# Kernel tuning notes

Measured on AMD Instinct MI355X. Metric: run time of the kernel, lower is better.

The kernel has to match this reference:

```python
import jax, jax.numpy as jnp
import numpy as np

EMB = 1024
HEADS = 16
HEAD_DIM = EMB // HEADS
FF = 4 * EMB
B, S = 4, 2048


def gelu_tanh(x):
    c = jnp.sqrt(jnp.asarray(2.0 / jnp.pi, x.dtype))
    return 0.5 * x * (1.0 + jnp.tanh(c * (x + 0.044715 * x ** 3)))


def layernorm(x, g, b, eps=1e-5):
    mu = jnp.mean(x, axis=-1, keepdims=True)
    var = jnp.var(x, axis=-1, keepdims=True)
    return (x - mu) * jax.lax.rsqrt(var + eps) * g + b


def setup_inputs() -> dict:
    key = jax.random.key(0)
    ks = jax.random.split(key, 12)
    s = 0.02
    return {
        "x": jax.random.normal(ks[0], (B, S, EMB), jnp.float32),
        "Wq": jax.random.normal(ks[1], (EMB, EMB), jnp.float32) * s,
        "bq": jnp.zeros((EMB,), jnp.float32),
        "Wk": jax.random.normal(ks[2], (EMB, EMB), jnp.float32) * s,
        "bk": jnp.zeros((EMB,), jnp.float32),
        "Wv": jax.random.normal(ks[3], (EMB, EMB), jnp.float32) * s,
        "bv": jnp.zeros((EMB,), jnp.float32),
        "Wo": jax.random.normal(ks[4], (EMB, EMB), jnp.float32) * s,
        "bo": jnp.zeros((EMB,), jnp.float32),
        "W1": jax.random.normal(ks[5], (EMB, FF), jnp.float32) * s,
        "b1": jnp.zeros((FF,), jnp.float32),
        "W2": jax.random.normal(ks[6], (FF, EMB), jnp.float32) * s,
        "b2": jnp.zeros((EMB,), jnp.float32),
        "g1": jnp.ones((EMB,), jnp.float32),
        "be1": jnp.zeros((EMB,), jnp.float32),
        "g2": jnp.ones((EMB,), jnp.float32),
        "be2": jnp.zeros((EMB,), jnp.float32),
    }


def reference(x, Wq, bq, Wk, bk, Wv, bv, Wo, bo, W1, b1, W2, b2, g1, be1, g2, be2):
    b, s, _ = x.shape
    shortcut = x
    h = layernorm(x, g1, be1)
    # QKV projections -> [b, heads, s, head_dim]
    def proj(W, bias):
        return (h @ W + bias).reshape(b, s, HEADS, HEAD_DIM).transpose(0, 2, 1, 3)
    q, k, v = proj(Wq, bq), proj(Wk, bk), proj(Wv, bv)
    scores = jnp.einsum('bhqd,bhkd->bhqk', q, k) / jnp.sqrt(jnp.asarray(HEAD_DIM, x.dtype))
    causal = jnp.triu(jnp.ones((s, s), bool), k=1)  # True above diagonal -> masked
    scores = jnp.where(causal, -jnp.inf, scores)
    probs = jax.nn.softmax(scores, axis=-1)  # dropout p=0 -> identity
    ctx = jnp.einsum('bhqk,bhkd->bhqd', probs, v).transpose(0, 2, 1, 3).reshape(b, s, EMB)
    attn_out = ctx @ Wo + bo
    x = attn_out + shortcut
    shortcut = x
    h = layernorm(x, g2, be2)
    ff = gelu_tanh(h @ W1 + b1) @ W2 + b2
    return ff + shortcut
```

## Files before the change

kernel.cpp:

```cpp
#include <hip/hip_runtime.h>
#include <hip/hip_bf16.h>

#define EMB 1024
#define HEADS 16
#define HDIM 64
#define FFDIM 4096
#define BSZ 4
#define SEQ 2048
#define MROWS (BSZ * SEQ)
#define QKVW 3072
#define VSTRIDE 2080

typedef __attribute__((ext_vector_type(8))) short bf16x8;
typedef __attribute__((ext_vector_type(4))) float f32x4;
typedef __attribute__((ext_vector_type(16))) float f32x16;
typedef __attribute__((ext_vector_type(4))) unsigned short u16x4;
typedef unsigned short u16;

__device__ __forceinline__ float bf2f(u16 u) {
  union { unsigned int i; float f; } c; c.i = ((unsigned int)u) << 16; return c.f;
}
__device__ __forceinline__ u16 f2bf(float f) {
  union { float f; unsigned int i; } c; c.f = f;
  unsigned int i = c.i + 0x7fff + ((c.i >> 16) & 1);
  return (u16)(i >> 16);
}
__device__ __forceinline__ unsigned fbits(float f) {
  union { float f; unsigned u; } c; c.f = f; return c.u;
}
__device__ __forceinline__ unsigned pk2(float e0, float e1) {
  return (fbits(e0) >> 16) | (fbits(e1) & 0xffff0000u);
}
__device__ __forceinline__ f32x16 zero16() {
  f32x16 z;
#pragma unroll
  for (int i = 0; i < 16; ++i) z[i] = 0.f;
  return z;
}
__device__ __forceinline__ void gload16(const u16* g, void* lds) {
  __builtin_amdgcn_global_load_lds(
      (const __attribute__((address_space(1))) void*)g,
      (__attribute__((address_space(3))) void*)lds, 16, 0, 0);
}

__global__ __launch_bounds__(256) void ln_kernel(
    const float* __restrict__ x, const float* __restrict__ g,
    const float* __restrict__ be, u16* __restrict__ out) {
  int w = threadIdx.x >> 6, l = threadIdx.x & 63;
  size_t row = (size_t)blockIdx.x * 4 + w;
  const float* xr = x + row * EMB;
  float f[4][4];
  float s = 0.f, s2 = 0.f;
#pragma unroll
  for (int c = 0; c < 4; ++c) {
    f32x4 v = *(const f32x4*)(xr + c * 256 + l * 4);
#pragma unroll
    for (int j = 0; j < 4; ++j) {
      f[c][j] = v[j];
      s += v[j];
      s2 += v[j] * v[j];
    }
  }
#pragma unroll
  for (int m = 1; m < 64; m <<= 1) {
    s  += __shfl_xor(s, m);
    s2 += __shfl_xor(s2, m);
  }
  float mu = s * (1.f / EMB);
  float var = s2 * (1.f / EMB) - mu * mu;
  float rs = rsqrtf(var + 1e-5f);
#pragma unroll
  for (int c = 0; c < 4; ++c) {
    u16x4 o;
#pragma unroll
    for (int j = 0; j < 4; ++j) {
      int col = c * 256 + l * 4 + j;
      o[j] = f2bf((f[c][j] - mu) * rs * g[col] + be[col]);
    }
    *(u16x4*)(out + row * EMB + c * 256 + l * 4) = o;
  }
}

__global__ __launch_bounds__(256) void transpose_cvt(
    const float* __restrict__ in, u16* __restrict__ out, int R, int C) {
  __shared__ u16 tile[32][33];
  int c0 = blockIdx.x * 32, r0 = blockIdx.y * 32;
  int tx = threadIdx.x, ty = threadIdx.y;
#pragma unroll
  for (int i = ty; i < 32; i += 8)
    tile[i][tx] = f2bf(in[(size_t)(r0 + i) * C + c0 + tx]);
  __syncthreads();
#pragma unroll
  for (int i = ty; i < 32; i += 8)
    out[(size_t)(c0 + i) * R + r0 + tx] = tile[tx][i];
}

__global__ __launch_bounds__(256) void concat_bias(
    const float* __restrict__ a, const float* __restrict__ b,
    const float* __restrict__ c, float* __restrict__ o) {
  int i = blockIdx.x * 256 + threadIdx.x;
  o[i] = i < 1024 ? a[i] : (i < 2048 ? b[i - 1024] : c[i - 2048]);
}

__global__ __launch_bounds__(256) void transpose_v(
    const u16* __restrict__ QKV, u16* __restrict__ Vt) {
  __shared__ u16 tile[32][33];
  int s0 = blockIdx.x * 32, d0 = blockIdx.y * 32, bh = blockIdx.z;
  int h = bh % HEADS, b = bh / HEADS;
  int tx = threadIdx.x, ty = threadIdx.y;
  const u16* src = QKV + (size_t)b * SEQ * QKVW + 2048 + h * HDIM;
  u16* dst = Vt + (size_t)bh * HDIM * VSTRIDE;
#pragma unroll
  for (int i = ty; i < 32; i += 8)
    tile[i][tx] = src[(size_t)(s0 + i) * QKVW + d0 + tx];
  __syncthreads();
#pragma unroll
  for (int i = ty; i < 32; i += 8)
    dst[(size_t)(d0 + i) * VSTRIDE + s0 + tx] = tile[tx][i];
}

__device__ __forceinline__ float gelu_f(float v) {
  float u = 1.5957691216057308f * (v + 0.044715f * v * v * v);
  return v / (1.f + __expf(-u));
}

template <int EPI, typename OT>
__global__ __launch_bounds__(256, 3) void gemm32(
    const u16* __restrict__ A, const u16* __restrict__ Bt,
    const float* __restrict__ bias, const float* __restrict__ res,
    OT* __restrict__ C, int N, int K) {
  __shared__ char lds[16384];
  int nbn = N >> 7;
  int cpx = gridDim.x >> 3;
  int bid = blockIdx.x;
  int logical = (bid & 7) * cpx + (bid >> 3);
  int mb = logical / nbn, nb = logical % nbn;
  int m0 = mb << 7, n0 = nb << 7;
  int t = threadIdx.x, w = t >> 6, l = t & 63;
  int wr = w >> 1, wc = w & 1;
  int l31 = l & 31, lh = l >> 5;
  int srow = (w << 4) + (l >> 2);
  int scol = (((l & 3) ^ ((srow >> 1) & 3)) << 3);
  char* dstA = lds + (w << 10);
  char* dstB = lds + 8192 + (w << 10);

  f32x16 acc[2][2] = {{zero16(), zero16()}, {zero16(), zero16()}};

  for (int k0 = 0; k0 < K; k0 += 32) {
    __syncthreads();
    gload16(A + (size_t)(m0 + srow) * K + k0 + scol, dstA);
    gload16(A + (size_t)(m0 + 64 + srow) * K + k0 + scol, dstA + 4096);
    gload16(Bt + (size_t)(n0 + srow) * K + k0 + scol, dstB);
    gload16(Bt + (size_t)(n0 + 64 + srow) * K + k0 + scol, dstB + 4096);
    __syncthreads();
    bf16x8 afr[2][2], bfr[2][2];
#pragma unroll
    for (int blk = 0; blk < 2; ++blk)
#pragma unroll
      for (int kk = 0; kk < 2; ++kk) {
        int ra = (wr << 6) + (blk << 5) + l31;
        int rb = (wc << 6) + (blk << 5) + l31;
        int pa = (((kk << 1) + lh) ^ ((ra >> 1) & 3)) << 4;
        int pb = (((kk << 1) + lh) ^ ((rb >> 1) & 3)) << 4;
        afr[blk][kk] = *(const bf16x8*)(lds + ra * 64 + pa);
        bfr[blk][kk] = *(const bf16x8*)(lds + 8192 + rb * 64 + pb);
      }
#pragma unroll
    for (int m = 0; m < 2; ++m)
#pragma unroll
      for (int n = 0; n < 2; ++n)
#pragma unroll
        for (int kk = 0; kk < 2; ++kk)
          acc[m][n] = __builtin_amdgcn_mfma_f32_32x32x16_bf16(
              afr[m][kk], bfr[n][kk], acc[m][n], 0, 0, 0);
  }

#pragma unroll
  for (int m = 0; m < 2; ++m)
#pragma unroll
    for (int n = 0; n < 2; ++n) {
      int col = n0 + (wc << 6) + (n << 5) + l31;
      float bcol = bias[col];
      int rbase = m0 + (wr << 6) + (m << 5) + (lh << 2);
#pragma unroll
      for (int reg = 0; reg < 16; ++reg) {
        int row = rbase + (reg & 3) + ((reg >> 2) << 3);
        float v = acc[m][n][reg] + bcol;
        if (EPI & 2) v = gelu_f(v);
        if (EPI & 1) v += res[(size_t)row * N + col];
        if (sizeof(OT) == 2)
          C[(size_t)row * N + col] = (OT)f2bf(v);
        else
          C[(size_t)row * N + col] = (OT)v;
      }
    }
}

#define QKT32(ACCS, QF)                                                     \
  do {                                                                      \
    ACCS = zero16();                                                        \
    _Pragma("unroll") for (int s_ = 0; s_ < 4; ++s_)                        \
        ACCS = __builtin_amdgcn_mfma_f32_32x32x16_bf16(kf[s_], QF[s_],      \
                                                       ACCS, 0, 0, 0);      \
  } while (0)

#define ATTN_STEP(ACCS, M, L, O0, O1, DIAG)                                 \
  do {                                                                      \
    float e_[16];                                                           \
    float tm = -1e30f;                                                      \
    _Pragma("unroll") for (int i = 0; i < 16; ++i) {                        \
      float sv = ACCS[i];                                                   \
      if (DIAG) {                                                           \
        int kvl = (i & 3) + 8 * (i >> 2) + 4 * g;                           \
        if (kvl > lq) sv = -1e30f;                                          \
      }                                                                     \
      e_[i] = sv;                                                           \
      tm = fmaxf(tm, sv);                                                   \
    }                                                                       \
    tm = fmaxf(tm, __shfl_xor(tm, 32));                                     \
    float nm = fmaxf(M, tm);                                                \
    if (!__all(tm <= M)) {                                                  \
      float scl = __expf(M - nm);                                           \
      L *= scl;                                                             \
      _Pragma("unroll") for (int i = 0; i < 16; ++i) {                      \
        O0[i] *= scl;                                                       \
        O1[i] *= scl;                                                       \
      }                                                                     \
    }                                                                       \
    M = nm;                                                                 \
    float ts = 0.f;                                                         \
    _Pragma("unroll") for (int i = 0; i < 16; ++i) {                        \
      e_[i] = __expf(e_[i] - nm);                                           \
      ts += e_[i];                                                          \
    }                                                                       \
    ts += __shfl_xor(ts, 32);                                               \
    L += ts;                                                                \
    _Pragma("unroll") for (int s_ = 0; s_ < 2; ++s_) {                      \
      unsigned plo0 = pk2(e_[8 * s_ + 0], e_[8 * s_ + 1]);                  \
      unsigned plo1 = pk2(e_[8 * s_ + 2], e_[8 * s_ + 3]);                  \
      unsigned phi0 = pk2(e_[8 * s_ + 4], e_[8 * s_ + 5]);                  \
      unsigned phi1 = pk2(e_[8 * s_ + 6], e_[8 * s_ + 7]);                  \
      unsigned recv0 = __shfl_xor(g ? plo0 : phi0, 32);                     \
      unsigned recv1 = __shfl_xor(g ? plo1 : phi1, 32);                     \
      union { unsigned u[4]; bf16x8 v; } pf_;                               \
      pf_.u[0] = g ? recv0 : plo0;                                          \
      pf_.u[1] = g ? recv1 : plo1;                                          \
      pf_.u[2] = g ? phi0 : recv0;                                          \
      pf_.u[3] = g ? phi1 : recv1;                                          \
      O0 = __builtin_amdgcn_mfma_f32_32x32x16_bf16(vf[0][s_], pf_.v, O0,    \
                                                   0, 0, 0);                \
      O1 = __builtin_amdgcn_mfma_f32_32x32x16_bf16(vf[1][s_], pf_.v, O1,    \
                                                   0, 0, 0);                \
    }                                                                       \
  } while (0)

#define LOAD_KV(KV0)                                                        \
  do {                                                                      \
    _Pragma("unroll") for (int s_ = 0; s_ < 4; ++s_)                        \
        kf[s_] = *(const bf16x8*)(Kp + (size_t)((KV0) + lq) * QKVW +        \
                                  s_ * 16 + g * 8);                         \
    _Pragma("unroll") for (int d_ = 0; d_ < 2; ++d_)                        \
        _Pragma("unroll") for (int s_ = 0; s_ < 2; ++s_)                    \
            vf[d_][s_] = *(const bf16x8*)(Vt +                              \
                (size_t)(d_ * 32 + lq) * VSTRIDE + (KV0) + s_ * 16 + g * 8);\
  } while (0)

#define WRITE_OUT(O0, O1, L, WQ0)                                           \
  do {                                                                      \
    float inv = 1.f / L;                                                    \
    u16* orow = Op + (size_t)((WQ0) + lq) * EMB;                            \
    _Pragma("unroll") for (int dblk = 0; dblk < 2; ++dblk) {                \
      _Pragma("unroll") for (int p = 0; p < 8; ++p) {                       \
        int i0 = 2 * p;                                                     \
        int d = dblk * 32 + 2 * (p & 1) + 8 * (p >> 1) + 4 * g;             \
        float v0 = (dblk ? O1[i0] : O0[i0]) * inv;                          \
        float v1 = (dblk ? O1[i0 + 1] : O0[i0 + 1]) * inv;                  \
        unsigned wd = (unsigned)f2bf(v0) | ((unsigned)f2bf(v1) << 16);      \
        *(unsigned*)(orow + d) = wd;                                        \
      }                                                                     \
    }                                                                       \
  } while (0)

__global__ __launch_bounds__(256, 2) void attn_kernel(
    const u16* __restrict__ QKV, const u16* __restrict__ VtG,
    u16* __restrict__ O) {
  int t = threadIdx.x, w = t >> 6, l = t & 63;
  int lq = l & 31, g = l >> 5;
  int wid = blockIdx.x * 4 + w;
  int qi = wid & 31, bh = wid >> 5;
  int h = bh & (HEADS - 1), b = bh >> 4;
  int wq0a = qi * 32, wq0b = (63 - qi) * 32;
  int ntA = qi + 1, ntB = 64 - qi;
  const u16* Qp = QKV + (size_t)b * SEQ * QKVW + h * HDIM;
  const u16* Kp = QKV + (size_t)b * SEQ * QKVW + 1024 + h * HDIM;
  const u16* Vt = VtG + (size_t)bh * HDIM * VSTRIDE;
  u16* Op = O + (size_t)b * SEQ * EMB + h * HDIM;

  bf16x8 qfA[4], qfB[4];
#pragma unroll
  for (int s = 0; s < 4; ++s) {
    bf16x8 ra = *(const bf16x8*)(Qp + (size_t)(wq0a + lq) * QKVW + s * 16 + g * 8);
    bf16x8 rb = *(const bf16x8*)(Qp + (size_t)(wq0b + lq) * QKVW + s * 16 + g * 8);
#pragma unroll
    for (int j = 0; j < 8; ++j) {
      qfA[s][j] = (short)f2bf(bf2f((u16)ra[j]) * 0.125f);
      qfB[s][j] = (short)f2bf(bf2f((u16)rb[j]) * 0.125f);
    }
  }

  f32x16 oA0 = zero16(), oA1 = zero16(), oB0 = zero16(), oB1 = zero16();
  f32x16 sA, sB;
  float mA = -1e30f, lA = 0.f, mB = -1e30f, lB = 0.f;
  bf16x8 kf[4], vf[2][2];

  for (int ti = 0; ti < ntA; ++ti) {
    int kv0 = ti * 32;
    LOAD_KV(kv0);
    QKT32(sA, qfA);
    QKT32(sB, qfB);
    bool diagA = (ti == ntA - 1);
    ATTN_STEP(sA, mA, lA, oA0, oA1, diagA);
    ATTN_STEP(sB, mB, lB, oB0, oB1, false);
  }
  WRITE_OUT(oA0, oA1, lA, wq0a);
  for (int ti = ntA; ti < ntB; ++ti) {
    int kv0 = ti * 32;
    LOAD_KV(kv0);
    QKT32(sB, qfB);
    bool diagB = (ti == ntB - 1);
    ATTN_STEP(sB, mB, lB, oB0, oB1, diagB);
  }
  WRITE_OUT(oB0, oB1, lB, wq0b);
}

extern "C" void kernel_launch(void* const* d_in, const int* in_sizes, int n_in,
                              void* d_out, int out_size, void* d_ws, size_t ws_size,
                              hipStream_t stream) {
  (void)in_sizes; (void)n_in; (void)out_size; (void)ws_size;
  const float* x   = (const float*)d_in[0];
  const float* Wq  = (const float*)d_in[1];
  const float* bq  = (const float*)d_in[2];
  const float* Wk  = (const float*)d_in[3];
  const float* bk  = (const float*)d_in[4];
  const float* Wv  = (const float*)d_in[5];
  const float* bv  = (const float*)d_in[6];
  const float* Wo  = (const float*)d_in[7];
  const float* bo  = (const float*)d_in[8];
  const float* W1  = (const float*)d_in[9];
  const float* b1  = (const float*)d_in[10];
  const float* W2  = (const float*)d_in[11];
  const float* b2  = (const float*)d_in[12];
  const float* g1  = (const float*)d_in[13];
  const float* be1 = (const float*)d_in[14];
  const float* g2  = (const float*)d_in[15];
  const float* be2 = (const float*)d_in[16];

  char* ws = (char*)d_ws;
  const size_t MB = 1ull << 20;
  u16*   WqkvT = (u16*)(ws + 0 * MB);
  u16*   WoT   = (u16*)(ws + 6 * MB);
  u16*   W1T   = (u16*)(ws + 8 * MB);
  u16*   W2T   = (u16*)(ws + 16 * MB);
  float* bqkv  = (float*)(ws + 24 * MB);
  u16*   hbuf  = (u16*)(ws + 25 * MB);
  float* x1f   = (float*)(ws + 41 * MB);
  u16*   qkv   = (u16*)(ws + 73 * MB);
  u16*   VtG   = (u16*)(ws + 121 * MB);
  u16*   gbuf  = (u16*)(ws + 73 * MB);

  dim3 tb(32, 8);
  transpose_cvt<<<dim3(EMB / 32, EMB / 32), tb, 0, stream>>>(Wq, WqkvT, EMB, EMB);
  transpose_cvt<<<dim3(EMB / 32, EMB / 32), tb, 0, stream>>>(Wk, WqkvT + 1024 * 1024, EMB, EMB);
  transpose_cvt<<<dim3(EMB / 32, EMB / 32), tb, 0, stream>>>(Wv, WqkvT + 2 * 1024 * 1024, EMB, EMB);
  transpose_cvt<<<dim3(EMB / 32, EMB / 32), tb, 0, stream>>>(Wo, WoT, EMB, EMB);
  transpose_cvt<<<dim3(FFDIM / 32, EMB / 32), tb, 0, stream>>>(W1, W1T, EMB, FFDIM);
  transpose_cvt<<<dim3(EMB / 32, FFDIM / 32), tb, 0, stream>>>(W2, W2T, FFDIM, EMB);
  concat_bias<<<12, 256, 0, stream>>>(bq, bk, bv, bqkv);

  ln_kernel<<<MROWS / 4, 256, 0, stream>>>(x, g1, be1, hbuf);

  gemm32<0, u16><<<(MROWS / 128) * (QKVW / 128), 256, 0, stream>>>(
      hbuf, WqkvT, bqkv, nullptr, qkv, QKVW, EMB);

  transpose_v<<<dim3(SEQ / 32, HDIM / 32, BSZ * HEADS), tb, 0, stream>>>(qkv, VtG);

  attn_kernel<<<BSZ * HEADS * (SEQ / 64) / 4, 256, 0, stream>>>(qkv, VtG, hbuf);

  gemm32<1, float><<<(MROWS / 128) * (EMB / 128), 256, 0, stream>>>(
      hbuf, WoT, bo, x, x1f, EMB, EMB);

  ln_kernel<<<MROWS / 4, 256, 0, stream>>>(x1f, g2, be2, hbuf);

  gemm32<2, u16><<<(MROWS / 128) * (FFDIM / 128), 256, 0, stream>>>(
      hbuf, W1T, b1, nullptr, gbuf, FFDIM, EMB);
  gemm32<1, float><<<(MROWS / 128) * (EMB / 128), 256, 0, stream>>>(
      gbuf, W2T, b2, x1f, (float*)d_out, EMB, FFDIM);
}
```

Baseline: 454.1 us.

## Restructure attention to one query tile per wave with double-buffered KV loads

Replaces the paired causal query tiles per wave (short plus long tile sharing K/V loads) with one 32-row query tile per wave, doubling the grid. K/V fragments are ping-pong double-buffered so the next tile's loads are issued before the current tile's MFMAs, s_setprio is raised around MFMA bursts, and launch bounds go to 3 waves per SIMD. This trades K/V load sharing between two tiles and built-in load balance for lower register pressure, more occupancy and load/compute overlap. Work per wave becomes uneven (1 to 64 tiles), which may create tail imbalance.

```diff
diff --git a/kernel.cpp b/kernel.cpp
--- a/kernel.cpp
+++ b/kernel.cpp
@@ -196,15 +196,17 @@
     }
 }
 
-#define QKT32(ACCS, QF)                                                     \
+#define QKT32A(ACCS, KF)                                                    \
   do {                                                                      \
     ACCS = zero16();                                                        \
+    __builtin_amdgcn_s_setprio(1);                                          \
     _Pragma("unroll") for (int s_ = 0; s_ < 4; ++s_)                        \
-        ACCS = __builtin_amdgcn_mfma_f32_32x32x16_bf16(kf[s_], QF[s_],      \
+        ACCS = __builtin_amdgcn_mfma_f32_32x32x16_bf16(KF[s_], qf[s_],      \
                                                        ACCS, 0, 0, 0);      \
+    __builtin_amdgcn_s_setprio(0);                                          \
   } while (0)
 
-#define ATTN_STEP(ACCS, M, L, O0, O1, DIAG)                                 \
+#define ATTN_STEPA(ACCS, VF, DIAG)                                          \
   do {                                                                      \
     float e_[16];                                                           \
     float tm = -1e30f;                                                      \
@@ -218,23 +220,23 @@
       tm = fmaxf(tm, sv);                                                   \
     }                                                                       \
     tm = fmaxf(tm, __shfl_xor(tm, 32));                                     \
-    float nm = fmaxf(M, tm);                                                \
-    if (!__all(tm <= M)) {                                                  \
-      float scl = __expf(M - nm);                                           \
-      L *= scl;                                                             \
+    float nm = fmaxf(mrun, tm);                                             \
+    if (!__all(tm <= mrun)) {                                               \
+      float scl = __expf(mrun - nm);                                        \
+      lrun *= scl;                                                          \
       _Pragma("unroll") for (int i = 0; i < 16; ++i) {                      \
-        O0[i] *= scl;                                                       \
-        O1[i] *= scl;                                                       \
+        o0[i] *= scl;                                                       \
+        o1[i] *= scl;                                                       \
       }                                                                     \
     }                                                                       \
-    M = nm;                                                                 \
+    mrun = nm;                                                              \
     float ts = 0.f;                                                         \
     _Pragma("unroll") for (int i = 0; i < 16; ++i) {                        \
       e_[i] = __expf(e_[i] - nm);                                           \
       ts += e_[i];                                                          \
     }                                                                       \
     ts += __shfl_xor(ts, 32);                                               \
-    L += ts;                                                                \
+    lrun += ts;                                                             \
     _Pragma("unroll") for (int s_ = 0; s_ < 2; ++s_) {                      \
       unsigned plo0 = pk2(e_[8 * s_ + 0], e_[8 * s_ + 1]);                  \
       unsigned plo1 = pk2(e_[8 * s_ + 2], e_[8 * s_ + 3]);                  \
@@ -247,90 +249,89 @@
       pf_.u[1] = g ? recv1 : plo1;                                          \
       pf_.u[2] = g ? phi0 : recv0;                                          \
       pf_.u[3] = g ? phi1 : recv1;                                          \
-      O0 = __builtin_amdgcn_mfma_f32_32x32x16_bf16(vf[0][s_], pf_.v, O0,    \
+      __builtin_amdgcn_s_setprio(1);                                        \
+      o0 = __builtin_amdgcn_mfma_f32_32x32x16_bf16(VF##0[s_], pf_.v, o0,    \
                                                    0, 0, 0);                \
-      O1 = __builtin_amdgcn_mfma_f32_32x32x16_bf16(vf[1][s_], pf_.v, O1,    \
+      o1 = __builtin_amdgcn_mfma_f32_32x32x16_bf16(VF##1[s_], pf_.v, o1,    \
                                                    0, 0, 0);                \
+      __builtin_amdgcn_s_setprio(0);                                        \
     }                                                                       \
   } while (0)
 
-#define LOAD_KV(KV0)                                                        \
+#define LOAD_KVA(KF, VF, KV0)                                               \
   do {                                                                      \
     _Pragma("unroll") for (int s_ = 0; s_ < 4; ++s_)                        \
-        kf[s_] = *(const bf16x8*)(Kp + (size_t)((KV0) + lq) * QKVW +        \
+        KF[s_] = *(const bf16x8*)(Kp + (size_t)((KV0) + lq) * QKVW +        \
                                   s_ * 16 + g * 8);                         \
-    _Pragma("unroll") for (int d_ = 0; d_ < 2; ++d_)                        \
-        _Pragma("unroll") for (int s_ = 0; s_ < 2; ++s_)                    \
-            vf[d_][s_] = *(const bf16x8*)(Vt +                              \
-                (size_t)(d_ * 32 + lq) * VSTRIDE + (KV0) + s_ * 16 + g * 8);\
+    _Pragma("unroll") for (int s_ = 0; s_ < 2; ++s_) {                      \
+      VF##0[s_] = *(const bf16x8*)(Vt + (size_t)lq * VSTRIDE + (KV0) +      \
+                                   s_ * 16 + g * 8);                        \
+      VF##1[s_] = *(const bf16x8*)(Vt + (size_t)(32 + lq) * VSTRIDE +       \
+                                   (KV0) + s_ * 16 + g * 8);                \
+    }                                                                       \
   } while (0)
 
-#define WRITE_OUT(O0, O1, L, WQ0)                                           \
-  do {                                                                      \
-    float inv = 1.f / L;                                                    \
-    u16* orow = Op + (size_t)((WQ0) + lq) * EMB;                            \
-    _Pragma("unroll") for (int dblk = 0; dblk < 2; ++dblk) {                \
-      _Pragma("unroll") for (int p = 0; p < 8; ++p) {                       \
-        int i0 = 2 * p;                                                     \
-        int d = dblk * 32 + 2 * (p & 1) + 8 * (p >> 1) + 4 * g;             \
-        float v0 = (dblk ? O1[i0] : O0[i0]) * inv;                          \
-        float v1 = (dblk ? O1[i0 + 1] : O0[i0 + 1]) * inv;                  \
-        unsigned wd = (unsigned)f2bf(v0) | ((unsigned)f2bf(v1) << 16);      \
-        *(unsigned*)(orow + d) = wd;                                        \
-      }                                                                     \
-    }                                                                       \
-  } while (0)
-
-__global__ __launch_bounds__(256, 2) void attn_kernel(
+__global__ __launch_bounds__(256, 3) void attn_kernel(
     const u16* __restrict__ QKV, const u16* __restrict__ VtG,
     u16* __restrict__ O) {
   int t = threadIdx.x, w = t >> 6, l = t & 63;
   int lq = l & 31, g = l >> 5;
   int wid = blockIdx.x * 4 + w;
-  int qi = wid & 31, bh = wid >> 5;
+  int qi = wid & 63, bh = wid >> 6;
   int h = bh & (HEADS - 1), b = bh >> 4;
-  int wq0a = qi * 32, wq0b = (63 - qi) * 32;
-  int ntA = qi + 1, ntB = 64 - qi;
+  int wq0 = (63 - qi) * 32;
+  int nt = 64 - qi;
   const u16* Qp = QKV + (size_t)b * SEQ * QKVW + h * HDIM;
   const u16* Kp = QKV + (size_t)b * SEQ * QKVW + 1024 + h * HDIM;
   const u16* Vt = VtG + (size_t)bh * HDIM * VSTRIDE;
   u16* Op = O + (size_t)b * SEQ * EMB + h * HDIM;
 
-  bf16x8 qfA[4], qfB[4];
+  bf16x8 qf[4];
 #pragma unroll
   for (int s = 0; s < 4; ++s) {
-    bf16x8 ra = *(const bf16x8*)(Qp + (size_t)(wq0a + lq) * QKVW + s * 16 + g * 8);
-    bf16x8 rb = *(const bf16x8*)(Qp + (size_t)(wq0b + lq) * QKVW + s * 16 + g * 8);
-#pragma unroll
-    for (int j = 0; j < 8; ++j) {
-      qfA[s][j] = (short)f2bf(bf2f((u16)ra[j]) * 0.125f);
-      qfB[s][j] = (short)f2bf(bf2f((u16)rb[j]) * 0.125f);
+    bf16x8 r = *(const bf16x8*)(Qp + (size_t)(wq0 + lq) * QKVW + s * 16 + g * 8);
+#pragma unroll
+    for (int j = 0; j < 8; ++j)
+      qf[s][j] = (short)f2bf(bf2f((u16)r[j]) * 0.125f);
+  }
+
+  f32x16 o0 = zero16(), o1 = zero16(), s;
+  float mrun = -1e30f, lrun = 0.f;
+  bf16x8 kfA[4], vfA0[2], vfA1[2], kfB[4], vfB0[2], vfB1[2];
+
+  LOAD_KVA(kfA, vfA, 0);
+  int ti = 0;
+  while (ti + 2 <= nt) {
+    LOAD_KVA(kfB, vfB, (ti + 1) * 32);
+    QKT32A(s, kfA);
+    ATTN_STEPA(s, vfA, false);
+    bool diagB = (ti + 2 == nt);
+    if (ti + 2 < nt) LOAD_KVA(kfA, vfA, (ti + 2) * 32);
+    QKT32A(s, kfB);
+    ATTN_STEPA(s, vfB, diagB);
+    ti += 2;
+  }
+  if (ti < nt) {
+    QKT32A(s, kfA);
+    ATTN_STEPA(s, vfA, true);
+  }
+
+  {
+    float inv = 1.f / lrun;
+    u16* orow = Op + (size_t)(wq0 + lq) * EMB;
+#pragma unroll
+    for (int dblk = 0; dblk < 2; ++dblk) {
+#pragma unroll
+      for (int p = 0; p < 8; ++p) {
+        int i0 = 2 * p;
+        int d = dblk * 32 + 2 * (p & 1) + 8 * (p >> 1) + 4 * g;
+        float v0 = (dblk ? o1[i0] : o0[i0]) * inv;
+        float v1 = (dblk ? o1[i0 + 1] : o0[i0 + 1]) * inv;
+        unsigned wd = (unsigned)f2bf(v0) | ((unsigned)f2bf(v1) << 16);
+        *(unsigned*)(orow + d) = wd;
+      }
     }
   }
-
-  f32x16 oA0 = zero16(), oA1 = zero16(), oB0 = zero16(), oB1 = zero16();
-  f32x16 sA, sB;
-  float mA = -1e30f, lA = 0.f, mB = -1e30f, lB = 0.f;
-  bf16x8 kf[4], vf[2][2];
-
-  for (int ti = 0; ti < ntA; ++ti) {
-    int kv0 = ti * 32;
-    LOAD_KV(kv0);
-    QKT32(sA, qfA);
-    QKT32(sB, qfB);
-    bool diagA = (ti == ntA - 1);
-    ATTN_STEP(sA, mA, lA, oA0, oA1, diagA);
-    ATTN_STEP(sB, mB, lB, oB0, oB1, false);
-  }
-  WRITE_OUT(oA0, oA1, lA, wq0a);
-  for (int ti = ntA; ti < ntB; ++ti) {
-    int kv0 = ti * 32;
-    LOAD_KV(kv0);
-    QKT32(sB, qfB);
-    bool diagB = (ti == ntB - 1);
-    ATTN_STEP(sB, mB, lB, oB0, oB1, diagB);
-  }
-  WRITE_OUT(oB0, oB1, lB, wq0b);
 }
 
 extern "C" void kernel_launch(void* const* d_in, const int* in_sizes, int n_in,
@@ -384,7 +385,7 @@
 
   transpose_v<<<dim3(SEQ / 32, HDIM / 32, BSZ * HEADS), tb, 0, stream>>>(qkv, VtG);
 
-  attn_kernel<<<BSZ * HEADS * (SEQ / 64) / 4, 256, 0, stream>>>(qkv, VtG, hbuf);
+  attn_kernel<<<BSZ * HEADS * (SEQ / 32) / 4, 256, 0, stream>>>(qkv, VtG, hbuf);
 
   gemm32<1, float><<<(MROWS / 128) * (EMB / 128), 256, 0, stream>>>(
       hbuf, WoT, bo, x, x1f, EMB, EMB);
```

New measurement: 539.6 us. 18.8% more time.

## Split attention KV range across wave pairs and double GEMM K-step

Applied to the files above, without the earlier changes.

The attention kernel now gives each query-tile pair to two waves that each process half of the KV tiles, then merges the partial softmax states through shared memory, doubling the grid and raising the occupancy hint. MFMA sections are wrapped in s_setprio raises. Separately, the GEMM loads a 64-wide K slab per iteration with an 8-way XOR swizzle, halving the barrier count at the cost of twice the LDS per block. The extra merge step, the shared-memory footprint and the larger LDS could reduce occupancy.

```diff
diff --git a/kernel.cpp b/kernel.cpp
--- a/kernel.cpp
+++ b/kernel.cpp
@@ -129,7 +129,9 @@
     const u16* __restrict__ A, const u16* __restrict__ Bt,
     const float* __restrict__ bias, const float* __restrict__ res,
     OT* __restrict__ C, int N, int K) {
-  __shared__ char lds[16384];
+  __shared__ char lds[32768];
+  char* ldsA = lds;
+  char* ldsB = lds + 16384;
   int nbn = N >> 7;
   int cpx = gridDim.x >> 3;
   int bid = blockIdx.x;
@@ -139,40 +141,44 @@
   int t = threadIdx.x, w = t >> 6, l = t & 63;
   int wr = w >> 1, wc = w & 1;
   int l31 = l & 31, lh = l >> 5;
-  int srow = (w << 4) + (l >> 2);
-  int scol = (((l & 3) ^ ((srow >> 1) & 3)) << 3);
-  char* dstA = lds + (w << 10);
-  char* dstB = lds + 8192 + (w << 10);
+  int srow8 = l >> 3, sp8 = l & 7;
 
   f32x16 acc[2][2] = {{zero16(), zero16()}, {zero16(), zero16()}};
 
-  for (int k0 = 0; k0 < K; k0 += 32) {
+  for (int k0 = 0; k0 < K; k0 += 64) {
     __syncthreads();
-    gload16(A + (size_t)(m0 + srow) * K + k0 + scol, dstA);
-    gload16(A + (size_t)(m0 + 64 + srow) * K + k0 + scol, dstA + 4096);
-    gload16(Bt + (size_t)(n0 + srow) * K + k0 + scol, dstB);
-    gload16(Bt + (size_t)(n0 + 64 + srow) * K + k0 + scol, dstB + 4096);
+#pragma unroll
+    for (int ps = 0; ps < 4; ++ps) {
+      int r = ps * 32 + (w << 3) + srow8;
+      int sc = (sp8 ^ (r & 7)) << 3;
+      gload16(A + (size_t)(m0 + r) * K + k0 + sc, ldsA + ps * 4096 + (w << 10));
+      gload16(Bt + (size_t)(n0 + r) * K + k0 + sc, ldsB + ps * 4096 + (w << 10));
+    }
     __syncthreads();
-    bf16x8 afr[2][2], bfr[2][2];
-#pragma unroll
-    for (int blk = 0; blk < 2; ++blk)
-#pragma unroll
-      for (int kk = 0; kk < 2; ++kk) {
-        int ra = (wr << 6) + (blk << 5) + l31;
-        int rb = (wc << 6) + (blk << 5) + l31;
-        int pa = (((kk << 1) + lh) ^ ((ra >> 1) & 3)) << 4;
-        int pb = (((kk << 1) + lh) ^ ((rb >> 1) & 3)) << 4;
-        afr[blk][kk] = *(const bf16x8*)(lds + ra * 64 + pa);
-        bfr[blk][kk] = *(const bf16x8*)(lds + 8192 + rb * 64 + pb);
-      }
-#pragma unroll
-    for (int m = 0; m < 2; ++m)
-#pragma unroll
-      for (int n = 0; n < 2; ++n)
-#pragma unroll
-        for (int kk = 0; kk < 2; ++kk)
-          acc[m][n] = __builtin_amdgcn_mfma_f32_32x32x16_bf16(
-              afr[m][kk], bfr[n][kk], acc[m][n], 0, 0, 0);
+#pragma unroll
+    for (int hf = 0; hf < 2; ++hf) {
+      bf16x8 afr[2][2], bfr[2][2];
+#pragma unroll
+      for (int blk = 0; blk < 2; ++blk)
+#pragma unroll
+        for (int kk = 0; kk < 2; ++kk) {
+          int kki = hf * 2 + kk;
+          int ra = (wr << 6) + (blk << 5) + l31;
+          int rb = (wc << 6) + (blk << 5) + l31;
+          int pa = (((kki << 1) + lh) ^ (ra & 7)) << 4;
+          int pb = (((kki << 1) + lh) ^ (rb & 7)) << 4;
+          afr[blk][kk] = *(const bf16x8*)(ldsA + ra * 128 + pa);
+          bfr[blk][kk] = *(const bf16x8*)(ldsB + rb * 128 + pb);
+        }
+#pragma unroll
+      for (int m = 0; m < 2; ++m)
+#pragma unroll
+        for (int n = 0; n < 2; ++n)
+#pragma unroll
+          for (int kk = 0; kk < 2; ++kk)
+            acc[m][n] = __builtin_amdgcn_mfma_f32_32x32x16_bf16(
+                afr[m][kk], bfr[n][kk], acc[m][n], 0, 0, 0);
+    }
   }
 
 #pragma unroll
@@ -196,15 +202,17 @@
     }
 }
 
-#define QKT32(ACCS, QF)                                                     \
+#define QKT(ACCS, QF)                                                       \
   do {                                                                      \
     ACCS = zero16();                                                        \
+    __builtin_amdgcn_s_setprio(1);                                          \
     _Pragma("unroll") for (int s_ = 0; s_ < 4; ++s_)                        \
         ACCS = __builtin_amdgcn_mfma_f32_32x32x16_bf16(kf[s_], QF[s_],      \
                                                        ACCS, 0, 0, 0);      \
+    __builtin_amdgcn_s_setprio(0);                                          \
   } while (0)
 
-#define ATTN_STEP(ACCS, M, L, O0, O1, DIAG)                                 \
+#define STEP(ACCS, M, L, O0, O1, DIAG)                                      \
   do {                                                                      \
     float e_[16];                                                           \
     float tm = -1e30f;                                                      \
@@ -247,50 +255,79 @@
       pf_.u[1] = g ? recv1 : plo1;                                          \
       pf_.u[2] = g ? phi0 : recv0;                                          \
       pf_.u[3] = g ? phi1 : recv1;                                          \
-      O0 = __builtin_amdgcn_mfma_f32_32x32x16_bf16(vf[0][s_], pf_.v, O0,    \
+      __builtin_amdgcn_s_setprio(1);                                        \
+      O0 = __builtin_amdgcn_mfma_f32_32x32x16_bf16(vf0[s_], pf_.v, O0,      \
                                                    0, 0, 0);                \
-      O1 = __builtin_amdgcn_mfma_f32_32x32x16_bf16(vf[1][s_], pf_.v, O1,    \
+      O1 = __builtin_amdgcn_mfma_f32_32x32x16_bf16(vf1[s_], pf_.v, O1,      \
                                                    0, 0, 0);                \
+      __builtin_amdgcn_s_setprio(0);                                        \
     }                                                                       \
   } while (0)
 
-#define LOAD_KV(KV0)                                                        \
+#define LOADKV(KV0)                                                         \
   do {                                                                      \
     _Pragma("unroll") for (int s_ = 0; s_ < 4; ++s_)                        \
         kf[s_] = *(const bf16x8*)(Kp + (size_t)((KV0) + lq) * QKVW +        \
                                   s_ * 16 + g * 8);                         \
-    _Pragma("unroll") for (int d_ = 0; d_ < 2; ++d_)                        \
-        _Pragma("unroll") for (int s_ = 0; s_ < 2; ++s_)                    \
-            vf[d_][s_] = *(const bf16x8*)(Vt +                              \
-                (size_t)(d_ * 32 + lq) * VSTRIDE + (KV0) + s_ * 16 + g * 8);\
+    _Pragma("unroll") for (int s_ = 0; s_ < 2; ++s_) {                      \
+      vf0[s_] = *(const bf16x8*)(Vt + (size_t)lq * VSTRIDE + (KV0) +        \
+                                 s_ * 16 + g * 8);                          \
+      vf1[s_] = *(const bf16x8*)(Vt + (size_t)(32 + lq) * VSTRIDE +         \
+                                 (KV0) + s_ * 16 + g * 8);                  \
+    }                                                                       \
   } while (0)
 
-#define WRITE_OUT(O0, O1, L, WQ0)                                           \
+#define STORE_PART(PO, PML, O0, O1, M, L)                                   \
   do {                                                                      \
-    float inv = 1.f / L;                                                    \
-    u16* orow = Op + (size_t)((WQ0) + lq) * EMB;                            \
-    _Pragma("unroll") for (int dblk = 0; dblk < 2; ++dblk) {                \
+    float* rp = (PO) + lq * 68;                                             \
+    _Pragma("unroll") for (int dblk = 0; dblk < 2; ++dblk)                  \
       _Pragma("unroll") for (int p = 0; p < 8; ++p) {                       \
         int i0 = 2 * p;                                                     \
         int d = dblk * 32 + 2 * (p & 1) + 8 * (p >> 1) + 4 * g;             \
-        float v0 = (dblk ? O1[i0] : O0[i0]) * inv;                          \
-        float v1 = (dblk ? O1[i0 + 1] : O0[i0 + 1]) * inv;                  \
+        float2 v2;                                                          \
+        v2.x = (dblk ? (O1)[i0] : (O0)[i0]);                                \
+        v2.y = (dblk ? (O1)[i0 + 1] : (O0)[i0 + 1]);                        \
+        *(float2*)(rp + d) = v2;                                            \
+      }                                                                     \
+    if (!g) { (PML)[lq * 2] = (M); (PML)[lq * 2 + 1] = (L); }               \
+  } while (0)
+
+#define MERGE_OUT(PO, PML, O0, O1, M, L, WQ0)                               \
+  do {                                                                      \
+    float* rp = (PO) + lq * 68;                                             \
+    float m1 = (PML)[lq * 2], l1 = (PML)[lq * 2 + 1];                       \
+    float mm = fmaxf((M), m1);                                              \
+    float sa = __expf((M) - mm), sb = __expf(m1 - mm);                      \
+    float inv = 1.f / ((L) * sa + l1 * sb);                                 \
+    u16* orow = Op + (size_t)((WQ0) + lq) * EMB;                            \
+    _Pragma("unroll") for (int dblk = 0; dblk < 2; ++dblk)                  \
+      _Pragma("unroll") for (int p = 0; p < 8; ++p) {                       \
+        int i0 = 2 * p;                                                     \
+        int d = dblk * 32 + 2 * (p & 1) + 8 * (p >> 1) + 4 * g;             \
+        float2 q2 = *(const float2*)(rp + d);                               \
+        float v0 = ((dblk ? (O1)[i0] : (O0)[i0]) * sa + q2.x * sb) * inv;   \
+        float v1 = ((dblk ? (O1)[i0 + 1] : (O0)[i0 + 1]) * sa + q2.y * sb)  \
+                   * inv;                                                   \
         unsigned wd = (unsigned)f2bf(v0) | ((unsigned)f2bf(v1) << 16);      \
         *(unsigned*)(orow + d) = wd;                                        \
       }                                                                     \
-    }                                                                       \
   } while (0)
 
-__global__ __launch_bounds__(256, 2) void attn_kernel(
+__global__ __launch_bounds__(256, 4) void attn_kernel(
     const u16* __restrict__ QKV, const u16* __restrict__ VtG,
     u16* __restrict__ O) {
+  __shared__ float po[2][2][32][68];
+  __shared__ float pml[2][2][32][2];
   int t = threadIdx.x, w = t >> 6, l = t & 63;
   int lq = l & 31, g = l >> 5;
-  int wid = blockIdx.x * 4 + w;
-  int qi = wid & 31, bh = wid >> 5;
+  int pp = w >> 1, sp = w & 1;
+  int pairId = blockIdx.x * 2 + pp;
+  int qi = pairId & 31, bh = pairId >> 5;
   int h = bh & (HEADS - 1), b = bh >> 4;
   int wq0a = qi * 32, wq0b = (63 - qi) * 32;
   int ntA = qi + 1, ntB = 64 - qi;
+  int half = (ntB + 1) >> 1;
+  int lo = sp ? half : 0, hi = sp ? ntB : half;
   const u16* Qp = QKV + (size_t)b * SEQ * QKVW + h * HDIM;
   const u16* Kp = QKV + (size_t)b * SEQ * QKVW + 1024 + h * HDIM;
   const u16* Vt = VtG + (size_t)bh * HDIM * VSTRIDE;
@@ -311,26 +348,31 @@
   f32x16 oA0 = zero16(), oA1 = zero16(), oB0 = zero16(), oB1 = zero16();
   f32x16 sA, sB;
   float mA = -1e30f, lA = 0.f, mB = -1e30f, lB = 0.f;
-  bf16x8 kf[4], vf[2][2];
-
-  for (int ti = 0; ti < ntA; ++ti) {
-    int kv0 = ti * 32;
-    LOAD_KV(kv0);
-    QKT32(sA, qfA);
-    QKT32(sB, qfB);
-    bool diagA = (ti == ntA - 1);
-    ATTN_STEP(sA, mA, lA, oA0, oA1, diagA);
-    ATTN_STEP(sB, mB, lB, oB0, oB1, false);
-  }
-  WRITE_OUT(oA0, oA1, lA, wq0a);
-  for (int ti = ntA; ti < ntB; ++ti) {
-    int kv0 = ti * 32;
-    LOAD_KV(kv0);
-    QKT32(sB, qfB);
-    bool diagB = (ti == ntB - 1);
-    ATTN_STEP(sB, mB, lB, oB0, oB1, diagB);
-  }
-  WRITE_OUT(oB0, oB1, lB, wq0b);
+  bf16x8 kf[4], vf0[2], vf1[2];
+
+  for (int ti = lo; ti < hi; ++ti) {
+    LOADKV(ti * 32);
+    if (ti < ntA) {
+      QKT(sA, qfA);
+      STEP(sA, mA, lA, oA0, oA1, ti == ntA - 1);
+    }
+    QKT(sB, qfB);
+    STEP(sB, mB, lB, oB0, oB1, ti == ntB - 1);
+  }
+
+  float* poA = &po[pp][0][0][0];
+  float* poB = &po[pp][1][0][0];
+  float* mlA = &pml[pp][0][0][0];
+  float* mlB = &pml[pp][1][0][0];
+  if (sp) {
+    STORE_PART(poA, mlA, oA0, oA1, mA, lA);
+    STORE_PART(poB, mlB, oB0, oB1, mB, lB);
+  }
+  __syncthreads();
+  if (!sp) {
+    MERGE_OUT(poA, mlA, oA0, oA1, mA, lA, wq0a);
+    MERGE_OUT(poB, mlB, oB0, oB1, mB, lB, wq0b);
+  }
 }
 
 extern "C" void kernel_launch(void* const* d_in, const int* in_sizes, int n_in,
@@ -384,7 +426,7 @@
 
   transpose_v<<<dim3(SEQ / 32, HDIM / 32, BSZ * HEADS), tb, 0, stream>>>(qkv, VtG);
 
-  attn_kernel<<<BSZ * HEADS * (SEQ / 64) / 4, 256, 0, stream>>>(qkv, VtG, hbuf);
+  attn_kernel<<<BSZ * HEADS * (SEQ / 64) / 2, 256, 0, stream>>>(qkv, VtG, hbuf);
 
   gemm32<1, float><<<(MROWS / 128) * (EMB / 128), 256, 0, stream>>>(
       hbuf, WoT, bo, x, x1f, EMB, EMB);
```

New measurement: 576.1 us. 1.27x slower.
